# Kernel optimization log

Hardware: AMD Instinct MI355X
Metric: run time of the kernel (lower is better)

Reference implementation:

```python
import jax, jax.numpy as jnp
import numpy as np

NUM_LINKS = 4096
BUDGET = 100.0      # total_power_budget
PMAX = 0.1          # per_link_max
N_BISECT = 60       # bisection iterations (fp32 converges well before this)


def setup_inputs() -> dict:
    key = jax.random.key(0)
    raw_power = jax.random.normal(key, (8192, NUM_LINKS), dtype=jnp.float32)
    return {"raw_power": raw_power}


def _project(raw):
    """Euclidean projection of each row of raw onto {p : 0<=p<=PMAX, sum(p)<=BUDGET}.

    Closed-form water-filling: if clip(raw,0,PMAX) is feasible it is the answer;
    otherwise p = clip(raw - tau, 0, PMAX) with tau chosen so sum(p) = BUDGET
    (found by batched bisection + one implicit-function Newton correction,
    which also gives the exact QP-projection Jacobian).
    """
    clipped = jnp.clip(raw, 0.0, PMAX)
    feasible = jnp.sum(clipped, axis=-1, keepdims=True) <= BUDGET  # (B,1)

    raw_sg = jax.lax.stop_gradient(raw)
    lo = jnp.min(raw_sg, axis=-1, keepdims=True) - PMAX  # g(lo) = n*PMAX >= BUDGET
    hi = jnp.max(raw_sg, axis=-1, keepdims=True)         # g(hi) = 0

    def body(_, lohi):
        lo, hi = lohi
        mid = 0.5 * (lo + hi)
        g = jnp.sum(jnp.clip(raw_sg - mid, 0.0, PMAX), axis=-1, keepdims=True)
        too_big = g > BUDGET  # tau must increase
        return (jnp.where(too_big, mid, lo), jnp.where(too_big, hi, mid))

    lo, hi = jax.lax.fori_loop(0, N_BISECT, body, (lo, hi))
    tau0 = 0.5 * (lo + hi)  # (B,1), no gradient

    # Implicit-function (Newton) correction: g(tau) = sum(clip(raw-tau,0,PMAX)) = BUDGET.
    # dg/dtau = -n_active, dg/draw_i = active_i  => dtau/draw_i = active_i / n_active.
    active = (raw_sg - tau0 > 0.0) & (raw_sg - tau0 < PMAX)
    n_active = jnp.maximum(jnp.sum(active, axis=-1, keepdims=True).astype(raw.dtype), 1.0)
    g0 = jnp.sum(jnp.clip(raw - tau0, 0.0, PMAX), axis=-1, keepdims=True)
    tau = tau0 + (g0 - BUDGET) / n_active  # value ~= tau0, correct gradient

    p_budget = jnp.clip(raw - tau, 0.0, PMAX)
    return jnp.where(feasible, clipped, p_budget)


def reference(raw_power) -> jnp.ndarray:
    return _project(raw_power)
```

## Files before the change

### kernel.cpp

```cpp
#include <hip/hip_runtime.h>

#define NLINKS 4096
#define CHUNKS 4

typedef float fvec4 __attribute__((ext_vector_type(4)));

constexpr float kPmax = 0.1f;
constexpr float kBudget = 100.0f;
constexpr int kGrid = 5;
constexpr float kBmax = 16.0f;
constexpr int kFallbackIters = 8;

__device__ __forceinline__ float clip01(float x) {
  return __builtin_amdgcn_fmed3f(x, 0.0f, kPmax);
}

template <int N>
__device__ __forceinline__ void waveReduceSumN(float* x) {
#pragma unroll
  for (int m = 32; m >= 1; m >>= 1) {
    float t[N];
#pragma unroll
    for (int k = 0; k < N; ++k) t[k] = __shfl_xor(x[k], m, 64);
#pragma unroll
    for (int k = 0; k < N; ++k) x[k] += t[k];
  }
}

__global__ __launch_bounds__(256) void proj_kernel(
    const float* __restrict__ raw, float* __restrict__ out, int rows) {
  const int row = blockIdx.x;
  if (row >= rows) return;
  const int tid = threadIdx.x;
  const int wave = tid >> 6;
  const int lane = tid & 63;

  __shared__ float ldsA[4][kGrid + 1];
  __shared__ float ldsF[4];
  __shared__ float ldsN[4][2];

  const fvec4* rp = (const fvec4*)(raw + (size_t)row * NLINKS);
  fvec4* op = (fvec4*)(out + (size_t)row * NLINKS);

  fvec4 v[CHUNKS];
#pragma unroll
  for (int j = 0; j < CHUNKS; ++j)
    v[j] = __builtin_nontemporal_load(&rp[tid + 256 * j]);

  const float pts[kGrid] = {0.54f, 0.60f, 0.65f, 0.70f, 0.76f};

  float s[kGrid + 1];
#pragma unroll
  for (int k = 0; k <= kGrid; ++k) s[k] = 0.f;
#pragma unroll
  for (int j = 0; j < CHUNKS; ++j) {
#pragma unroll
    for (int c = 0; c < 4; ++c) {
      const float x = v[j][c];
      s[0] += clip01(x);
#pragma unroll
      for (int i = 0; i < kGrid; ++i) s[i + 1] += clip01(x - pts[i]);
    }
  }
  waveReduceSumN<kGrid + 1>(s);
  if (lane == 0) {
#pragma unroll
    for (int k = 0; k <= kGrid; ++k) ldsA[wave][k] = s[k];
  }
  __syncthreads();
#pragma unroll
  for (int k = 0; k <= kGrid; ++k)
    s[k] = (ldsA[0][k] + ldsA[1][k]) + (ldsA[2][k] + ldsA[3][k]);
  const float fs = s[0];

  if (fs <= kBudget) {
#pragma unroll
    for (int j = 0; j < CHUNKS; ++j) {
      fvec4 o;
#pragma unroll
      for (int c = 0; c < 4; ++c) o[c] = clip01(v[j][c]);
      __builtin_nontemporal_store(o, &op[tid + 256 * j]);
    }
    return;
  }

  float a = 0.f, ga = fs, b = kBmax, gb = 0.f;
  bool need_iter = true;
  if (s[1] < kBudget) {
    a = 0.f; ga = fs; b = pts[0]; gb = s[1];
  } else if (s[kGrid] > kBudget) {
    a = pts[kGrid - 1]; ga = s[kGrid]; b = kBmax; gb = 0.f;
  } else {
#pragma unroll
    for (int i = 0; i < kGrid - 1; ++i) {
      if (s[i + 1] >= kBudget && s[i + 2] <= kBudget) {
        a = pts[i]; ga = s[i + 1]; b = pts[i + 1]; gb = s[i + 2];
        need_iter = false;
        break;
      }
    }
  }

  if (need_iter) {
    int side = 0;
#pragma unroll 1
    for (int it = 0; it < kFallbackIters; ++it) {
      const float denom = gb - ga;
      float t = (denom != 0.f) ? b - (gb - kBudget) * (b - a) / denom
                               : 0.5f * (a + b);
      if (!(t > a && t < b)) t = 0.5f * (a + b);
      float s0 = 0.f, s1 = 0.f, s2 = 0.f, s3 = 0.f;
#pragma unroll
      for (int j = 0; j < CHUNKS; ++j) {
        s0 += clip01(v[j].x - t);
        s1 += clip01(v[j].y - t);
        s2 += clip01(v[j].z - t);
        s3 += clip01(v[j].w - t);
      }
      float g = (s0 + s1) + (s2 + s3);
      waveReduceSumN<1>(&g);
      if (lane == 0) ldsF[wave] = g;
      __syncthreads();
      g = (ldsF[0] + ldsF[1]) + (ldsF[2] + ldsF[3]);
      __syncthreads();
      if (g > kBudget) {
        a = t; ga = g;
        if (side == 1) gb = kBudget + 0.5f * (gb - kBudget);
        side = 1;
      } else {
        b = t; gb = g;
        if (side == -1) ga = kBudget + 0.5f * (ga - kBudget);
        side = -1;
      }
    }
  }

  const float dd = ga - gb;
  float tau0 = (dd != 0.f) ? a + (ga - kBudget) * (b - a) / dd : 0.5f * (a + b);
  if (!(tau0 >= a && tau0 <= b)) tau0 = 0.5f * (a + b);

  float gn[2] = {0.f, 0.f};
#pragma unroll
  for (int j = 0; j < CHUNKS; ++j) {
#pragma unroll
    for (int c = 0; c < 4; ++c) {
      const float t = v[j][c] - tau0;
      gn[0] += clip01(t);
      gn[1] += (t > 0.f && t < kPmax) ? 1.f : 0.f;
    }
  }
  waveReduceSumN<2>(gn);
  if (lane == 0) {
    ldsN[wave][0] = gn[0];
    ldsN[wave][1] = gn[1];
  }
  __syncthreads();
  gn[0] = (ldsN[0][0] + ldsN[1][0]) + (ldsN[2][0] + ldsN[3][0]);
  gn[1] = (ldsN[0][1] + ldsN[1][1]) + (ldsN[2][1] + ldsN[3][1]);
  const float tau = tau0 + (gn[0] - kBudget) / fmaxf(gn[1], 1.0f);

#pragma unroll
  for (int j = 0; j < CHUNKS; ++j) {
    fvec4 o;
#pragma unroll
    for (int c = 0; c < 4; ++c) o[c] = clip01(v[j][c] - tau);
    __builtin_nontemporal_store(o, &op[tid + 256 * j]);
  }
}

extern "C" void kernel_launch(void* const* d_in, const int* in_sizes, int n_in,
                              void* d_out, int out_size, void* d_ws, size_t ws_size,
                              hipStream_t stream) {
  const float* raw = (const float*)d_in[0];
  float* out = (float*)d_out;
  const int rows = in_sizes[0] / NLINKS;
  hipLaunchKernelGGL(proj_kernel, dim3(rows), dim3(256), 0, stream,
                     raw, out, rows);
}
```

Baseline: 220.5 us.

## Process four rows per block with double-buffered register prefetch of next row

```diff
diff --git a/kernel.cpp b/kernel.cpp
--- a/kernel.cpp
+++ b/kernel.cpp
@@ -2,6 +2,7 @@
 
 #define NLINKS 4096
 #define CHUNKS 4
+#define RPB 4
 
 typedef float fvec4 __attribute__((ext_vector_type(4)));
 
@@ -27,25 +28,32 @@
   }
 }
 
-__global__ __launch_bounds__(256) void proj_kernel(
-    const float* __restrict__ raw, float* __restrict__ out, int rows) {
-  const int row = blockIdx.x;
-  if (row >= rows) return;
-  const int tid = threadIdx.x;
-  const int wave = tid >> 6;
-  const int lane = tid & 63;
-
-  __shared__ float ldsA[4][kGrid + 1];
-  __shared__ float ldsF[4];
-  __shared__ float ldsN[4][2];
-
+__device__ __forceinline__ void ldsBarrier() {
+  asm volatile("s_waitcnt lgkmcnt(0)" ::: "memory");
+  __builtin_amdgcn_s_barrier();
+  asm volatile("" ::: "memory");
+}
+
+struct SharedBufs {
+  float A[2][4][kGrid + 1];
+  float N[2][4][2];
+  float F[4];
+};
+
+__device__ __forceinline__ void loadRow(const float* __restrict__ raw, int row,
+                                        int tid, fvec4 (&v)[CHUNKS]) {
   const fvec4* rp = (const fvec4*)(raw + (size_t)row * NLINKS);
-  fvec4* op = (fvec4*)(out + (size_t)row * NLINKS);
-
-  fvec4 v[CHUNKS];
 #pragma unroll
   for (int j = 0; j < CHUNKS; ++j)
     v[j] = __builtin_nontemporal_load(&rp[tid + 256 * j]);
+}
+
+template <int P>
+__device__ __forceinline__ void processRow(const fvec4 (&v)[CHUNKS],
+                                           float* __restrict__ out, int row,
+                                           int tid, int wave, int lane,
+                                           SharedBufs& sh) {
+  fvec4* op = (fvec4*)(out + (size_t)row * NLINKS);
 
   const float pts[kGrid] = {0.54f, 0.60f, 0.65f, 0.70f, 0.76f};
 
@@ -65,12 +73,12 @@
   waveReduceSumN<kGrid + 1>(s);
   if (lane == 0) {
 #pragma unroll
-    for (int k = 0; k <= kGrid; ++k) ldsA[wave][k] = s[k];
-  }
-  __syncthreads();
+    for (int k = 0; k <= kGrid; ++k) sh.A[P][wave][k] = s[k];
+  }
+  ldsBarrier();
 #pragma unroll
   for (int k = 0; k <= kGrid; ++k)
-    s[k] = (ldsA[0][k] + ldsA[1][k]) + (ldsA[2][k] + ldsA[3][k]);
+    s[k] = (sh.A[P][0][k] + sh.A[P][1][k]) + (sh.A[P][2][k] + sh.A[P][3][k]);
   const float fs = s[0];
 
   if (fs <= kBudget) {
@@ -119,9 +127,9 @@
       }
       float g = (s0 + s1) + (s2 + s3);
       waveReduceSumN<1>(&g);
-      if (lane == 0) ldsF[wave] = g;
+      if (lane == 0) sh.F[wave] = g;
       __syncthreads();
-      g = (ldsF[0] + ldsF[1]) + (ldsF[2] + ldsF[3]);
+      g = (sh.F[0] + sh.F[1]) + (sh.F[2] + sh.F[3]);
       __syncthreads();
       if (g > kBudget) {
         a = t; ga = g;
@@ -151,12 +159,12 @@
   }
   waveReduceSumN<2>(gn);
   if (lane == 0) {
-    ldsN[wave][0] = gn[0];
-    ldsN[wave][1] = gn[1];
-  }
-  __syncthreads();
-  gn[0] = (ldsN[0][0] + ldsN[1][0]) + (ldsN[2][0] + ldsN[3][0]);
-  gn[1] = (ldsN[0][1] + ldsN[1][1]) + (ldsN[2][1] + ldsN[3][1]);
+    sh.N[P][wave][0] = gn[0];
+    sh.N[P][wave][1] = gn[1];
+  }
+  ldsBarrier();
+  gn[0] = (sh.N[P][0][0] + sh.N[P][1][0]) + (sh.N[P][2][0] + sh.N[P][3][0]);
+  gn[1] = (sh.N[P][0][1] + sh.N[P][1][1]) + (sh.N[P][2][1] + sh.N[P][3][1]);
   const float tau = tau0 + (gn[0] - kBudget) / fmaxf(gn[1], 1.0f);
 
 #pragma unroll
@@ -166,6 +174,28 @@
     for (int c = 0; c < 4; ++c) o[c] = clip01(v[j][c] - tau);
     __builtin_nontemporal_store(o, &op[tid + 256 * j]);
   }
+}
+
+__global__ __launch_bounds__(256) void proj_kernel(
+    const float* __restrict__ raw, float* __restrict__ out, int rows) {
+  __shared__ SharedBufs sh;
+  const int tid = threadIdx.x;
+  const int wave = tid >> 6;
+  const int lane = tid & 63;
+  const int r0 = blockIdx.x * RPB;
+  if (r0 >= rows) return;
+
+  fvec4 vA[CHUNKS], vB[CHUNKS];
+  const bool h1 = r0 + 1 < rows, h2 = r0 + 2 < rows, h3 = r0 + 3 < rows;
+
+  loadRow(raw, r0, tid, vA);
+  if (h1) loadRow(raw, r0 + 1, tid, vB);
+  processRow<0>(vA, out, r0, tid, wave, lane, sh);
+  if (h2) loadRow(raw, r0 + 2, tid, vA);
+  if (h1) processRow<1>(vB, out, r0 + 1, tid, wave, lane, sh);
+  if (h3) loadRow(raw, r0 + 3, tid, vB);
+  if (h2) processRow<0>(vA, out, r0 + 2, tid, wave, lane, sh);
+  if (h3) processRow<1>(vB, out, r0 + 3, tid, wave, lane, sh);
 }
 
 extern "C" void kernel_launch(void* const* d_in, const int* in_sizes, int n_in,
@@ -174,6 +204,7 @@
   const float* raw = (const float*)d_in[0];
   float* out = (float*)d_out;
   const int rows = in_sizes[0] / NLINKS;
-  hipLaunchKernelGGL(proj_kernel, dim3(rows), dim3(256), 0, stream,
+  const int blocks = (rows + RPB - 1) / RPB;
+  hipLaunchKernelGGL(proj_kernel, dim3(blocks), dim3(256), 0, stream,
                      raw, out, rows);
 }
```

New measurement: 222.4 us. Within noise of the previous version (+0.9%).

## Split projection into a per-row tau kernel and a separate apply kernel

Applied to the files above, without the earlier changes.

```diff
diff --git a/kernel.cpp b/kernel.cpp
--- a/kernel.cpp
+++ b/kernel.cpp
@@ -27,8 +27,9 @@
   }
 }
 
-__global__ __launch_bounds__(256) void proj_kernel(
-    const float* __restrict__ raw, float* __restrict__ out, int rows) {
+
+__global__ __launch_bounds__(256) void tau_kernel(
+    const float* __restrict__ raw, float* __restrict__ tau_out, int rows) {
   const int row = blockIdx.x;
   if (row >= rows) return;
   const int tid = threadIdx.x;
@@ -40,12 +41,10 @@
   __shared__ float ldsN[4][2];
 
   const fvec4* rp = (const fvec4*)(raw + (size_t)row * NLINKS);
-  fvec4* op = (fvec4*)(out + (size_t)row * NLINKS);
 
   fvec4 v[CHUNKS];
 #pragma unroll
-  for (int j = 0; j < CHUNKS; ++j)
-    v[j] = __builtin_nontemporal_load(&rp[tid + 256 * j]);
+  for (int j = 0; j < CHUNKS; ++j) v[j] = rp[tid + 256 * j];
 
   const float pts[kGrid] = {0.54f, 0.60f, 0.65f, 0.70f, 0.76f};
 
@@ -74,13 +73,7 @@
   const float fs = s[0];
 
   if (fs <= kBudget) {
-#pragma unroll
-    for (int j = 0; j < CHUNKS; ++j) {
-      fvec4 o;
-#pragma unroll
-      for (int c = 0; c < 4; ++c) o[c] = clip01(v[j][c]);
-      __builtin_nontemporal_store(o, &op[tid + 256 * j]);
-    }
+    if (tid == 0) tau_out[row] = 0.f;
     return;
   }
 
@@ -159,12 +152,25 @@
   gn[1] = (ldsN[0][1] + ldsN[1][1]) + (ldsN[2][1] + ldsN[3][1]);
   const float tau = tau0 + (gn[0] - kBudget) / fmaxf(gn[1], 1.0f);
 
+  if (tid == 0) tau_out[row] = tau;
+}
+
+__global__ __launch_bounds__(256) void apply_kernel(
+    const float* __restrict__ raw, const float* __restrict__ tau_arr,
+    float* __restrict__ out, int rows) {
+  const int tid = threadIdx.x;
+  for (int row = blockIdx.x; row < rows; row += gridDim.x) {
+    const float tau = tau_arr[row];
+    const fvec4* rp = (const fvec4*)(raw + (size_t)row * NLINKS);
+    fvec4* op = (fvec4*)(out + (size_t)row * NLINKS);
 #pragma unroll
-  for (int j = 0; j < CHUNKS; ++j) {
-    fvec4 o;
+    for (int j = 0; j < CHUNKS; ++j) {
+      const fvec4 x = rp[tid + 256 * j];
+      fvec4 o;
 #pragma unroll
-    for (int c = 0; c < 4; ++c) o[c] = clip01(v[j][c] - tau);
-    __builtin_nontemporal_store(o, &op[tid + 256 * j]);
+      for (int c = 0; c < 4; ++c) o[c] = clip01(x[c] - tau);
+      __builtin_nontemporal_store(o, &op[tid + 256 * j]);
+    }
   }
 }
 
@@ -174,6 +180,11 @@
   const float* raw = (const float*)d_in[0];
   float* out = (float*)d_out;
   const int rows = in_sizes[0] / NLINKS;
-  hipLaunchKernelGGL(proj_kernel, dim3(rows), dim3(256), 0, stream,
-                     raw, out, rows);
+  float* tau_arr = (float*)d_ws;
+
+  hipLaunchKernelGGL(tau_kernel, dim3(rows), dim3(256), 0, stream,
+                     raw, tau_arr, rows);
+  int blocks = rows < 2048 ? rows : 2048;
+  hipLaunchKernelGGL(apply_kernel, dim3(blocks), dim3(256), 0, stream,
+                     raw, tau_arr, out, rows);
 }
```

Result: slower. 246.5 us (+11.8%).
